# Kernel tuning notes

Measured on AMD Instinct MI355X. Metric: run time of the kernel, lower is better.

Reference implementation:

```python
import jax, jax.numpy as jnp
import numpy as np

B, C_IN, C_OUT, T, N, KS = 16, 64, 64, 48, 1024, 3

def setup_inputs() -> dict:
    key = jax.random.key(0)
    k1, k2, k3, k4 = jax.random.split(key, 4)
    x = jax.random.normal(k1, (B, C_IN, T, N), dtype=jnp.float32)
    Lk = jax.random.normal(k2, (KS, N, N), dtype=jnp.float32) / np.sqrt(N)
    # kaiming-uniform-like init for theta, uniform for b
    fan_in = C_IN * KS
    bound_t = np.sqrt(6.0 / fan_in)
    theta = jax.random.uniform(k3, (C_IN, C_OUT, KS), dtype=jnp.float32,
                               minval=-bound_t, maxval=bound_t)
    bound_b = 1.0 / np.sqrt(fan_in)
    b = jax.random.uniform(k4, (1, C_OUT, 1, 1), dtype=jnp.float32,
                           minval=-bound_b, maxval=bound_b)
    return {"x": x, "Lk": Lk, "theta": theta, "b": b}

def reference(x, Lk, theta, b):
    # x: [B, c_in, T, N], Lk: [ks, N, N], theta: [c_in, c_out, ks], b: [1, c_out, 1, 1]
    x_c = jnp.einsum('knm,bitm->bitkn', Lk, x)          # [B, c_in, T, ks, N]
    x_gc = jnp.einsum('iok,bitkn->botn', theta, x_c) + b  # [B, c_out, T, N]
    # Align: c_in == c_out -> identity
    return jax.nn.relu(x_gc + x)
```

## Files before the change

### kernel.cpp

```cpp
#include <hip/hip_runtime.h>
#include <hip/hip_bf16.h>
#include <stdint.h>


typedef short bs8 __attribute__((ext_vector_type(8)));
typedef float f32x4 __attribute__((ext_vector_type(4)));

#define NB   16
#define NC   64
#define NT   48
#define NN   1024
#define NKS  3
#define KDIM 3072
#define KT   48

__device__ __forceinline__ short f2bs(float f) {
  uint32_t u = __builtin_bit_cast(uint32_t, f);
  u = (u + 0x7FFFu + ((u >> 16) & 1u)) >> 16;
  return (short)u;
}

__device__ __forceinline__ void gload16(const void* g, void* l) {
  __builtin_amdgcn_global_load_lds(
      (const __attribute__((address_space(1))) void*)g,
      (__attribute__((address_space(3))) void*)l, 16, 0, 0);
}

__global__ __launch_bounds__(256) void k_prep_bt(const float* __restrict__ Lk,
                                                 short* __restrict__ BT) {
  int gid = blockIdx.x * 256 + threadIdx.x;
  int e = gid * 4;
  int k = e >> 20;
  int rem = e & 1048575;
  int n = rem >> 10;
  int m = rem & 1023;
  float4 v = *reinterpret_cast<const float4*>(Lk + e);
  union { short s[4]; uint64_t u; } p;
  p.s[0] = f2bs(v.x); p.s[1] = f2bs(v.y); p.s[2] = f2bs(v.z); p.s[3] = f2bs(v.w);
  *reinterpret_cast<uint64_t*>(BT + (size_t)n * KDIM + k * NN + m) = p.u;
}

__global__ __launch_bounds__(256, 2) void k_step1(const float* __restrict__ x,
                                                  const float* __restrict__ theta,
                                                  short* __restrict__ Y, int b0) {
  __shared__ __align__(16) short th[NKS * 64 * 72];
  __shared__ __align__(16) float xs[64 * 128];
  int tid = threadIdx.x;
  int wave = tid >> 6;
  for (int idx = tid; idx < NC * NC * NKS; idx += 256) {
    int i = idx / (NC * NKS);
    int r = idx - i * (NC * NKS);
    int o = r / NKS;
    int k = r - o * NKS;
    th[(k * 64 + o) * 72 + i] = f2bs(theta[idx]);
  }

  int bid = blockIdx.x;
  int mt  = bid & 7;
  int btl = bid >> 3;
  int b_l = btl / NT;
  int t   = btl - b_l * NT;
  int b   = b0 + b_l;
  const float* xb = x + (size_t)b * (NC * NT * NN) + (size_t)t * NN + mt * 128;

#pragma unroll
  for (int c = 0; c < 8; ++c) {
    int idx = c * 256 + tid;
    int row = idx >> 5, ch = idx & 31;
    gload16(xb + (size_t)row * (NT * NN) + ch * 4,
            xs + (c * 256 + wave * 64) * 4);
  }
  __syncthreads();

  int lane = tid & 63;
  int l15 = lane & 15, lg = lane >> 4;
  size_t yrow0 = (size_t)btl * 64;

  for (int nni = 0; nni < 2; ++nni) {
    int mloc = wave * 32 + nni * 16 + l15;
    float xv[16];
#pragma unroll
    for (int j = 0; j < 16; ++j) {
      int i = ((j >> 3) << 5) + lg * 8 + (j & 7);
      xv[j] = xs[i * 128 + mloc];
    }
    f32x4 acc[3][4];
#pragma unroll
    for (int k = 0; k < 3; ++k)
#pragma unroll
      for (int mi = 0; mi < 4; ++mi)
        acc[k][mi] = (f32x4){0.f, 0.f, 0.f, 0.f};

#pragma unroll
    for (int ks = 0; ks < 2; ++ks) {
      bs8 bfrag;
#pragma unroll
      for (int j = 0; j < 8; ++j) bfrag[j] = f2bs(xv[ks * 8 + j]);
#pragma unroll
      for (int mi = 0; mi < 4; ++mi) {
#pragma unroll
        for (int k = 0; k < 3; ++k) {
          const bs8* ap = reinterpret_cast<const bs8*>(
              &th[(k * 64 + mi * 16 + l15) * 72 + ks * 32 + lg * 8]);
          acc[k][mi] = __builtin_amdgcn_mfma_f32_16x16x32_bf16(
              *ap, bfrag, acc[k][mi], 0, 0, 0);
        }
      }
    }
    int mcol = mt * 128 + mloc;
#pragma unroll
    for (int k = 0; k < 3; ++k)
#pragma unroll
      for (int mi = 0; mi < 4; ++mi)
#pragma unroll
        for (int q = 0; q < 4; ++q) {
          int o = mi * 16 + lg * 4 + q;
          Y[(yrow0 + o) * KDIM + k * NN + mcol] = f2bs(acc[k][mi][q]);
        }
  }
}


__device__ __forceinline__ void stage_half(const short* __restrict__ src,
                                           short* lds, int h, int tid) {
  int wave = tid >> 6;
#pragma unroll
  for (int r = 0; r < 2; ++r) {
    int idx = h * 1024 + r * 512 + tid;
    int row = idx >> 3, c8 = idx & 7;
    int c8s = c8 ^ (row & 7);
    gload16(src + (size_t)row * KDIM + c8s * 8,
            lds + (h * 1024 + r * 512 + wave * 64) * 8);
  }
}

#define VMC(N) asm volatile("s_waitcnt vmcnt(" #N ")" ::: "memory")
#define BARR() __builtin_amdgcn_s_barrier();

#define READ_A(DST, QM, P)                                                \
  _Pragma("unroll") for (int e = 0; e < 4; ++e)                           \
    _Pragma("unroll") for (int ks = 0; ks < 2; ++ks) {                    \
      int rw = (8 * (QM) + 2 * e + wr) * 16 + l15;                        \
      DST[e][ks] = *(const bs8*)&AL[(P) * 16384 + rw * 64 +               \
                    ((ks * 32 + lg * 8) ^ ((rw & 7) << 3))];              \
    }

#define READ_B(DST, QN, P)                                                \
  _Pragma("unroll") for (int f = 0; f < 2; ++f)                           \
    _Pragma("unroll") for (int ks = 0; ks < 2; ++ks) {                    \
      int rw = (8 * (QN) + 4 * f + wc) * 16 + l15;                        \
      DST[f][ks] = *(const bs8*)&BL[(P) * 16384 + rw * 64 +               \
                    ((ks * 32 + lg * 8) ^ ((rw & 7) << 3))];              \
    }

#define COMPUTE(QM, AF, BF, QN)                                             \
  __builtin_amdgcn_s_setprio(1);                                            \
  _Pragma("unroll") for (int ks = 0; ks < 2; ++ks)                          \
    _Pragma("unroll") for (int e = 0; e < 4; ++e)                           \
      _Pragma("unroll") for (int f = 0; f < 2; ++f)                         \
        acc[4 * (QM) + e][2 * (QN) + f] =                                   \
            __builtin_amdgcn_mfma_f32_16x16x32_bf16(                        \
                AF[e][ks], BF[f][ks], acc[4 * (QM) + e][2 * (QN) + f],      \
                0, 0, 0);                                                   \
  __builtin_amdgcn_s_setprio(0);

#define TILE(t, P, S1, S2, VM)                                              \
  {                                                                         \
    bs8 af[4][2], bf0[2][2], bf1[2][2];                                     \
    READ_A(af, 0, P);                                                       \
    READ_B(bf0, 0, P);                                                      \
    if (S1) stage_half(Yb + ((t) + 1) * 64, AL + ((P) ^ 1) * 16384, 1, tid);\
    BARR();                                                                 \
    COMPUTE(0, af, bf0, 0);                                                 \
    READ_B(bf1, 1, P);                                                      \
    if (S1) stage_half(BTb + ((t) + 1) * 64, BL + ((P) ^ 1) * 16384, 1, tid);\
    BARR();                                                                 \
    COMPUTE(0, af, bf1, 1);                                                 \
    READ_A(af, 1, P);                                                       \
    if (S2) stage_half(Yb + ((t) + 2) * 64, AL + (P) * 16384, 0, tid);      \
    BARR();                                                                 \
    COMPUTE(1, af, bf1, 1);                                                 \
    if (S2) stage_half(BTb + ((t) + 2) * 64, BL + (P) * 16384, 0, tid);     \
    VM;                                                                     \
    BARR();                                                                 \
    COMPUTE(1, af, bf0, 0);                                                 \
  }

__global__ __launch_bounds__(512, 2) void k_gemm(const short* __restrict__ Y,
                                                 const short* __restrict__ BT,
                                                 const float* __restrict__ x,
                                                 const float* __restrict__ bias,
                                                 float* __restrict__ out,
                                                 int b0, int nwg) {
  __shared__ __align__(16) short AL[2 * 16384];
  __shared__ __align__(16) short BL[2 * 16384];

  int bid = blockIdx.x;
  int cpx = nwg >> 3;
  int swz = (bid & 7) * cpx + (bid >> 3);
  int colb = swz & 3;
  int rowb = swz >> 2;

  int tid = threadIdx.x;
  int lane = tid & 63, wave = tid >> 6;
  int wr = wave >> 2, wc = wave & 3;
  int l15 = lane & 15, lg = lane >> 4;
  int row0 = rowb * 256, col0 = colb * 256;

  const short* Yb  = Y  + (size_t)row0 * KDIM;
  const short* BTb = BT + (size_t)col0 * KDIM;

  f32x4 acc[8][4];
#pragma unroll
  for (int j = 0; j < 8; ++j)
#pragma unroll
    for (int i = 0; i < 4; ++i) acc[j][i] = (f32x4){0.f, 0.f, 0.f, 0.f};

  stage_half(Yb,        AL,         0, tid);
  stage_half(Yb,        AL,         1, tid);
  stage_half(BTb,       BL,         0, tid);
  stage_half(BTb,       BL,         1, tid);
  stage_half(Yb + 64,   AL + 16384, 0, tid);
  stage_half(BTb + 64,  BL + 16384, 0, tid);
  VMC(4);
  BARR();

  for (int t = 0; t < KT - 2; t += 2) {
    TILE(t,     0, 1, 1, VMC(4));
    TILE(t + 1, 1, 1, 1, VMC(4));
  }
  TILE(KT - 2, 0, 1, 0, VMC(0));
  TILE(KT - 1, 1, 0, 0, (void)0);

#pragma unroll
  for (int j = 0; j < 8; ++j) {
#pragma unroll
    for (int q = 0; q < 4; ++q) {
      int r = row0 + (2 * j + wr) * 16 + lg * 4 + q;
      int o = r & 63;
      int btl = r >> 6;
      int tt = btl % NT;
      int bb = b0 + btl / NT;
      float bo = bias[o];
      size_t obase = ((size_t)(bb * 64 + o) * NT + tt) * NN;
#pragma unroll
      for (int i = 0; i < 4; ++i) {
        int n = col0 + (4 * i + wc) * 16 + l15;
        size_t oidx = obase + n;
        float v = acc[j][i][q] + bo + x[oidx];
        out[oidx] = v > 0.f ? v : 0.f;
      }
    }
  }
}

extern "C" void kernel_launch(void* const* d_in, const int* in_sizes, int n_in,
                              void* d_out, int out_size, void* d_ws, size_t ws_size,
                              hipStream_t stream) {
  const float* x     = (const float*)d_in[0];
  const float* Lk    = (const float*)d_in[1];
  const float* theta = (const float*)d_in[2];
  const float* bias  = (const float*)d_in[3];
  float* out = (float*)d_out;

  char* ws = (char*)d_ws;
  short* BT = (short*)ws;
  short* Y  = (short*)(ws + (size_t)(8u << 20));
  size_t avail = ws_size > ((size_t)8u << 20) ? ws_size - ((size_t)8u << 20) : 0;
  size_t perB = (size_t)NT * NC * KDIM * 2;
  int bc = 16;
  while (bc > 1 && (size_t)bc * perB > avail) bc >>= 1;

  k_prep_bt<<<dim3(3072), dim3(256), 0, stream>>>(Lk, BT);
  for (int b0 = 0; b0 < NB; b0 += bc) {
    k_step1<<<dim3(bc * 384), dim3(256), 0, stream>>>(x, theta, Y, b0);
    int nwg = bc * 48;
    k_gemm<<<dim3(nwg), dim3(512), 0, stream>>>(Y, BT, x, bias, out, b0, nwg);
  }
}
```

Before: 485.7 us.

## Switch main GEMM to 32x32x16 bf16 MFMA with extended LDS swizzle

Replaces the 16x16x32 MFMA tiling with 32x32x16 MFMA instructions. Each wave now holds 2x2 32x32 accumulator blocks per quadrant, so fewer MFMA issues and fewer LDS fragment reads are needed per tile. The LDS XOR swizzle gains an extra term on row bits 3-4 to avoid bank conflicts under the new 32-row read pattern, and the epilogue row/column mapping is rewritten for the 32x32 output layout. The risk is a different register footprint and a longer MFMA latency interacting with the existing barrier schedule.

```diff
diff --git a/kernel.cpp b/kernel.cpp
--- a/kernel.cpp
+++ b/kernel.cpp
@@ -5,6 +5,7 @@
 
 typedef short bs8 __attribute__((ext_vector_type(8)));
 typedef float f32x4 __attribute__((ext_vector_type(4)));
+typedef float f32x16 __attribute__((ext_vector_type(16)));
 
 #define NB   16
 #define NC   64
@@ -128,7 +129,7 @@
   for (int r = 0; r < 2; ++r) {
     int idx = h * 1024 + r * 512 + tid;
     int row = idx >> 3, c8 = idx & 7;
-    int c8s = c8 ^ (row & 7);
+    int c8s = c8 ^ (row & 7) ^ ((row >> 3) & 3);
     gload16(src + (size_t)row * KDIM + c8s * 8,
             lds + (h * 1024 + r * 512 + wave * 64) * 8);
   }
@@ -137,53 +138,49 @@
 #define VMC(N) asm volatile("s_waitcnt vmcnt(" #N ")" ::: "memory")
 #define BARR() __builtin_amdgcn_s_barrier();
 
-#define READ_A(DST, QM, P)                                                \
-  _Pragma("unroll") for (int e = 0; e < 4; ++e)                           \
-    _Pragma("unroll") for (int ks = 0; ks < 2; ++ks) {                    \
-      int rw = (8 * (QM) + 2 * e + wr) * 16 + l15;                        \
-      DST[e][ks] = *(const bs8*)&AL[(P) * 16384 + rw * 64 +               \
-                    ((ks * 32 + lg * 8) ^ ((rw & 7) << 3))];              \
-    }
-
-#define READ_B(DST, QN, P)                                                \
-  _Pragma("unroll") for (int f = 0; f < 2; ++f)                           \
-    _Pragma("unroll") for (int ks = 0; ks < 2; ++ks) {                    \
-      int rw = (8 * (QN) + 4 * f + wc) * 16 + l15;                        \
-      DST[f][ks] = *(const bs8*)&BL[(P) * 16384 + rw * 64 +               \
-                    ((ks * 32 + lg * 8) ^ ((rw & 7) << 3))];              \
-    }
-
-#define COMPUTE(QM, AF, BF, QN)                                             \
+#define READ_A32(DST, MP, P)                                                \
+  _Pragma("unroll") for (int e = 0; e < 2; ++e)                             \
+    _Pragma("unroll") for (int ks = 0; ks < 4; ++ks) {                      \
+      int row = (4 * (MP) + 2 * e + wr) * 32 + l31;                         \
+      int ch = (2 * ks + hi) ^ (row & 7) ^ ((row >> 3) & 3);                \
+      DST[e][ks] = *(const bs8*)&AL[(P) * 16384 + row * 64 + ch * 8];       \
+    }
+
+#define READ_B32(DST, NI, P)                                                \
+  _Pragma("unroll") for (int ks = 0; ks < 4; ++ks) {                        \
+    int row = (4 * (NI) + wc) * 32 + l31;                                   \
+    int ch = (2 * ks + hi) ^ (row & 7) ^ ((row >> 3) & 3);                  \
+    DST[ks] = *(const bs8*)&BL[(P) * 16384 + row * 64 + ch * 8];            \
+  }
+
+#define COMPUTE32(MP, BF, NI)                                               \
   __builtin_amdgcn_s_setprio(1);                                            \
-  _Pragma("unroll") for (int ks = 0; ks < 2; ++ks)                          \
-    _Pragma("unroll") for (int e = 0; e < 4; ++e)                           \
-      _Pragma("unroll") for (int f = 0; f < 2; ++f)                         \
-        acc[4 * (QM) + e][2 * (QN) + f] =                                   \
-            __builtin_amdgcn_mfma_f32_16x16x32_bf16(                        \
-                AF[e][ks], BF[f][ks], acc[4 * (QM) + e][2 * (QN) + f],      \
-                0, 0, 0);                                                   \
+  _Pragma("unroll") for (int ks = 0; ks < 4; ++ks)                          \
+    _Pragma("unroll") for (int e = 0; e < 2; ++e)                           \
+      acc[2 * (MP) + e][(NI)] = __builtin_amdgcn_mfma_f32_32x32x16_bf16(    \
+          af[e][ks], BF[ks], acc[2 * (MP) + e][(NI)], 0, 0, 0);             \
   __builtin_amdgcn_s_setprio(0);
 
 #define TILE(t, P, S1, S2, VM)                                              \
   {                                                                         \
-    bs8 af[4][2], bf0[2][2], bf1[2][2];                                     \
-    READ_A(af, 0, P);                                                       \
-    READ_B(bf0, 0, P);                                                      \
+    bs8 af[2][4], bf0[4], bf1[4];                                           \
+    READ_A32(af, 0, P);                                                     \
+    READ_B32(bf0, 0, P);                                                    \
     if (S1) stage_half(Yb + ((t) + 1) * 64, AL + ((P) ^ 1) * 16384, 1, tid);\
     BARR();                                                                 \
-    COMPUTE(0, af, bf0, 0);                                                 \
-    READ_B(bf1, 1, P);                                                      \
+    COMPUTE32(0, bf0, 0);                                                   \
+    READ_B32(bf1, 1, P);                                                    \
     if (S1) stage_half(BTb + ((t) + 1) * 64, BL + ((P) ^ 1) * 16384, 1, tid);\
     BARR();                                                                 \
-    COMPUTE(0, af, bf1, 1);                                                 \
-    READ_A(af, 1, P);                                                       \
+    COMPUTE32(0, bf1, 1);                                                   \
+    READ_A32(af, 1, P);                                                     \
     if (S2) stage_half(Yb + ((t) + 2) * 64, AL + (P) * 16384, 0, tid);      \
     BARR();                                                                 \
-    COMPUTE(1, af, bf1, 1);                                                 \
+    COMPUTE32(1, bf1, 1);                                                   \
     if (S2) stage_half(BTb + ((t) + 2) * 64, BL + (P) * 16384, 0, tid);     \
     VM;                                                                     \
     BARR();                                                                 \
-    COMPUTE(1, af, bf0, 0);                                                 \
+    COMPUTE32(1, bf0, 0);                                                   \
   }
 
 __global__ __launch_bounds__(512, 2) void k_gemm(const short* __restrict__ Y,
@@ -204,17 +201,19 @@
   int tid = threadIdx.x;
   int lane = tid & 63, wave = tid >> 6;
   int wr = wave >> 2, wc = wave & 3;
-  int l15 = lane & 15, lg = lane >> 4;
+  int l31 = lane & 31, hi = lane >> 5;
   int row0 = rowb * 256, col0 = colb * 256;
 
   const short* Yb  = Y  + (size_t)row0 * KDIM;
   const short* BTb = BT + (size_t)col0 * KDIM;
 
-  f32x4 acc[8][4];
-#pragma unroll
-  for (int j = 0; j < 8; ++j)
-#pragma unroll
-    for (int i = 0; i < 4; ++i) acc[j][i] = (f32x4){0.f, 0.f, 0.f, 0.f};
+  f32x16 acc[4][2];
+#pragma unroll
+  for (int a = 0; a < 4; ++a)
+#pragma unroll
+    for (int i = 0; i < 2; ++i)
+#pragma unroll
+      for (int q = 0; q < 16; ++q) acc[a][i][q] = 0.f;
 
   stage_half(Yb,        AL,         0, tid);
   stage_half(Yb,        AL,         1, tid);
@@ -233,10 +232,11 @@
   TILE(KT - 1, 1, 0, 0, (void)0);
 
 #pragma unroll
-  for (int j = 0; j < 8; ++j) {
-#pragma unroll
-    for (int q = 0; q < 4; ++q) {
-      int r = row0 + (2 * j + wr) * 16 + lg * 4 + q;
+  for (int a = 0; a < 4; ++a) {
+    int mf = 2 * a + wr;
+#pragma unroll
+    for (int q = 0; q < 16; ++q) {
+      int r = row0 + mf * 32 + (q & 3) + 8 * (q >> 2) + 4 * hi;
       int o = r & 63;
       int btl = r >> 6;
       int tt = btl % NT;
@@ -244,10 +244,10 @@
       float bo = bias[o];
       size_t obase = ((size_t)(bb * 64 + o) * NT + tt) * NN;
 #pragma unroll
-      for (int i = 0; i < 4; ++i) {
-        int n = col0 + (4 * i + wc) * 16 + l15;
+      for (int i = 0; i < 2; ++i) {
+        int n = col0 + (4 * i + wc) * 32 + l31;
         size_t oidx = obase + n;
-        float v = acc[j][i][q] + bo + x[oidx];
+        float v = acc[a][i][q] + bo + x[oidx];
         out[oidx] = v > 0.f ? v : 0.f;
       }
     }
```

Result: no change. 483.5 us (-0.5%).
